# Performance work log

Measured on AMD Instinct MI355X. Metric: run time of the kernel, lower is better.

## Reference

```python
import jax, jax.numpy as jnp
import numpy as np

B, T, C, H = 4, 2048, 1024, 16
HD = C // H

def setup_inputs() -> dict:
    key = jax.random.key(0)
    ks = jax.random.split(key, 9)
    s = 1.0 / np.sqrt(C)
    return {
        'x':  jax.random.normal(ks[0], (B, T, C), jnp.float32),
        'Wq': jax.random.normal(ks[1], (C, C), jnp.float32) * s,
        'bq': jnp.zeros((C,), jnp.float32),
        'Wk': jax.random.normal(ks[2], (C, C), jnp.float32) * s,
        'bk': jnp.zeros((C,), jnp.float32),
        'Wv': jax.random.normal(ks[3], (C, C), jnp.float32) * s,
        'bv': jnp.zeros((C,), jnp.float32),
        'Wo': jax.random.normal(ks[4], (C, C), jnp.float32) * s,
        'bo': jnp.zeros((C,), jnp.float32),
    }

def reference(x, Wq, bq, Wk, bk, Wv, bv, Wo, bo):
    Bx, Tx, Cx = x.shape
    # projections (torch Linear: x @ W.T + b); split heads -> (B,H,T,HD)
    def heads(y):
        return y.reshape(Bx, Tx, H, HD).transpose(0, 2, 1, 3)
    q = heads(x @ Wq.T + bq)
    k = heads(x @ Wk.T + bk)
    v = heads(x @ Wv.T + bv)
    # NOTE: original scales by 1/sqrt(embedding_dim), not head_dim
    scale = 1.0 / jnp.sqrt(jnp.asarray(Cx, x.dtype))
    att = jnp.einsum('bhqd,bhkd->bhqk', q, k) * scale
    mask = jnp.tril(jnp.ones((Tx, Tx), dtype=bool))
    att = jnp.where(mask, att, jnp.asarray(-jnp.inf, att.dtype))
    att = jax.nn.softmax(att, axis=-1)
    y = jnp.einsum('bhqk,bhkd->bhqd', att, v)
    y = y.transpose(0, 2, 1, 3).reshape(Bx, Tx, Cx)
    return y @ Wo.T + bo
```

## Files before the change

### kernel.cpp

```cpp
#include <hip/hip_runtime.h>
#include <hip/hip_bf16.h>
#include <stdint.h>

#define NB 4
#define NT 2048
#define NC 1024
#define NH 16
#define NHD 64
#define NM (NB*NT)

typedef __attribute__((ext_vector_type(8))) __bf16 bf16x8;
typedef __attribute__((ext_vector_type(4))) float floatx4;
typedef __attribute__((ext_vector_type(8))) unsigned short ushortx8;

#define AS1(p) ((const __attribute__((address_space(1))) void*)(p))
#define AS3(p) ((__attribute__((address_space(3))) void*)(p))

__device__ __forceinline__ unsigned short f2bf(float f) {
    union { float f; unsigned int u; } v; v.f = f;
    unsigned int u = v.u;
    return (unsigned short)((u + 0x7FFFu + ((u >> 16) & 1u)) >> 16);
}


__global__ void cast_x_tiled(const float* __restrict__ in,
                             unsigned short* __restrict__ out, int ntiles) {
    const int wid  = (blockIdx.x * blockDim.x + threadIdx.x) >> 6;
    const int lane = threadIdx.x & 63;
    if (wid >= ntiles) return;
    const int R = wid >> 5, C = wid & 31;
    const float* src = in + ((size_t)(R*16 + (lane >> 2)))*1024 + C*32 + (lane & 3)*8;
    const floatx4 v0 = *(const floatx4*)src;
    const floatx4 v1 = *(const floatx4*)(src + 4);
    ushortx8 o;
    o[0] = f2bf(v0[0]); o[1] = f2bf(v0[1]); o[2] = f2bf(v0[2]); o[3] = f2bf(v0[3]);
    o[4] = f2bf(v1[0]); o[5] = f2bf(v1[1]); o[6] = f2bf(v1[2]); o[7] = f2bf(v1[3]);
    *(ushortx8*)&out[(size_t)wid*512 + (((lane & 3)*16 + (lane >> 2)))*8] = o;
}

__global__ void cast4_tiled(const float* __restrict__ w0, const float* __restrict__ w1,
                            const float* __restrict__ w2, const float* __restrict__ w3,
                            unsigned short* __restrict__ o0, unsigned short* __restrict__ o1,
                            unsigned short* __restrict__ o2, unsigned short* __restrict__ o3,
                            int ntiles) {
    const int wid  = (blockIdx.x * blockDim.x + threadIdx.x) >> 6;
    const int lane = threadIdx.x & 63;
    if (wid >= ntiles) return;
    const float* in; unsigned short* out;
    switch (blockIdx.y) {
        case 0: in = w0; out = o0; break;
        case 1: in = w1; out = o1; break;
        case 2: in = w2; out = o2; break;
        default: in = w3; out = o3; break;
    }
    const int R = wid >> 5, C = wid & 31;
    const float* src = in + ((size_t)(R*16 + (lane >> 2)))*1024 + C*32 + (lane & 3)*8;
    const floatx4 v0 = *(const floatx4*)src;
    const floatx4 v1 = *(const floatx4*)(src + 4);
    ushortx8 o;
    o[0] = f2bf(v0[0]); o[1] = f2bf(v0[1]); o[2] = f2bf(v0[2]); o[3] = f2bf(v0[3]);
    o[4] = f2bf(v1[0]); o[5] = f2bf(v1[1]); o[6] = f2bf(v1[2]); o[7] = f2bf(v1[3]);
    *(ushortx8*)&out[(size_t)wid*512 + (((lane & 3)*16 + (lane >> 2)))*8] = o;
}

#define TM 128
#define TN 128
#define BK 32

__device__ __forceinline__ void gemm_core(
    const unsigned short* __restrict__ A,
    const unsigned short* __restrict__ W,
    const float* __restrict__ bias,
    void* __restrict__ Out,
    unsigned short* As, unsigned short* Bs,
    int m_base, int n_base, int N_out, int K, int mode, float oscale)
{
    const int tid  = threadIdx.x;
    const int lane = tid & 63;
    const int wv   = tid >> 6;
    const int quad = lane >> 4;
    const int l16  = lane & 15;
    const int wm = (wv >> 1) * 64;
    const int wn = (wv & 1) * 64;

    floatx4 acc[4][4];
    #pragma unroll
    for (int i = 0; i < 4; ++i)
        #pragma unroll
        for (int j = 0; j < 4; ++j)
            acc[i][j] = (floatx4){0.f, 0.f, 0.f, 0.f};

    const int kTiles = K / BK;
    const int kct = K >> 5;

    const unsigned short* At = A + ((size_t)((m_base >> 4) + wv*2) * kct) * 512 + (size_t)lane*8;
    const unsigned short* Wt = W + ((size_t)((n_base >> 4) + wv*2) * kct) * 512 + (size_t)lane*8;
    const size_t rstride = (size_t)kct * 512;

    for (int kt = 0; kt < kTiles; ++kt) {
        __syncthreads();
        #pragma unroll
        for (int i = 0; i < 2; ++i) {
            __builtin_amdgcn_global_load_lds(
                AS1(At + (size_t)kt*512 + i*rstride),
                AS3(&As[(wv*2 + i)*512]), 16, 0, 0);
            __builtin_amdgcn_global_load_lds(
                AS1(Wt + (size_t)kt*512 + i*rstride),
                AS3(&Bs[(wv*2 + i)*512]), 16, 0, 0);
        }
        __syncthreads();

        bf16x8 af[4], bfr[4];
        #pragma unroll
        for (int mi = 0; mi < 4; ++mi)
            af[mi] = *(const bf16x8*)&As[((wv >> 1)*4 + mi)*512 + lane*8];
        #pragma unroll
        for (int ni = 0; ni < 4; ++ni)
            bfr[ni] = *(const bf16x8*)&Bs[((wv & 1)*4 + ni)*512 + lane*8];

        #pragma unroll
        for (int mi = 0; mi < 4; ++mi)
            #pragma unroll
            for (int ni = 0; ni < 4; ++ni)
                acc[mi][ni] = __builtin_amdgcn_mfma_f32_16x16x32_bf16(
                    af[mi], bfr[ni], acc[mi][ni], 0, 0, 0);
    }

    #pragma unroll
    for (int mi = 0; mi < 4; ++mi) {
        #pragma unroll
        for (int ni = 0; ni < 4; ++ni) {
            const int col = n_base + wn + ni*16 + l16;
            const float bv = bias[col & 1023];
            #pragma unroll
            for (int r = 0; r < 4; ++r) {
                const int row = m_base + wm + mi*16 + quad*4 + r;
                const float v = (acc[mi][ni][r] + bv) * oscale;
                if (mode == 0) {
                    ((float*)Out)[(size_t)row * N_out + col] = v;
                } else if (mode == 1) {
                    const int bb = row >> 11, t = row & (NT - 1);
                    const int h  = (col >> 6) & (NH - 1), d = col & 63;
                    const int bh = bb * NH + h;
                    const size_t idx =
                        ((size_t)((bh*128 + (t >> 4))*2 + (d >> 5)))*512
                        + (size_t)((((d >> 3) & 3)*16 + (t & 15))*8 + (d & 7));
                    ((unsigned short*)Out)[idx] = f2bf(v);
                } else {
                    const int bb = row >> 11, t = row & (NT - 1);
                    const int h  = (col >> 6) & (NH - 1), hd = col & 63;
                    const int bh = bb * NH + h;
                    const size_t idx =
                        ((size_t)((bh*64 + (t >> 5))*4 + (hd >> 4)))*512
                        + (size_t)((((t >> 3) & 3)*16 + (hd & 15))*8 + (t & 7));
                    ((unsigned short*)Out)[idx] = f2bf(v);
                }
            }
        }
    }
}

#define QSCALE (0.03125f * 1.44269504088896340736f)

__global__ __launch_bounds__(256) void gemm_qkv(
    const unsigned short* __restrict__ A,
    const unsigned short* __restrict__ Wq, const unsigned short* __restrict__ Wk,
    const unsigned short* __restrict__ Wv,
    const float* __restrict__ bq, const float* __restrict__ bk,
    const float* __restrict__ bv,
    unsigned short* __restrict__ Qo, unsigned short* __restrict__ Ko,
    unsigned short* __restrict__ Vo)
{
    __shared__ __align__(16) unsigned short As[TM*BK];
    __shared__ __align__(16) unsigned short Bs[TN*BK];
    const int wi = blockIdx.y >> 3;
    const int n_base = (blockIdx.y & 7) * TN;
    const unsigned short* W; const float* bias; void* Out; int mode; float osc;
    if (wi == 0)      { W = Wq; bias = bq; Out = Qo; mode = 1; osc = QSCALE; }
    else if (wi == 1) { W = Wk; bias = bk; Out = Ko; mode = 1; osc = 1.0f; }
    else              { W = Wv; bias = bv; Out = Vo; mode = 2; osc = 1.0f; }
    gemm_core(A, W, bias, Out, As, Bs, blockIdx.x * TM, n_base, NC, NC, mode, osc);
}

__global__ __launch_bounds__(256) void gemm_out(
    const unsigned short* __restrict__ A,
    const unsigned short* __restrict__ W,
    const float* __restrict__ bias,
    float* __restrict__ Out)
{
    __shared__ __align__(16) unsigned short As[TM*BK];
    __shared__ __align__(16) unsigned short Bs[TN*BK];
    gemm_core(A, W, bias, Out, As, Bs, blockIdx.x * TM, blockIdx.y * TN,
              NC, NC, 0, 1.0f);
}

#define LDPP 68

__device__ __forceinline__ void attn_q32(
    const unsigned short* __restrict__ Qf,
    const unsigned short* __restrict__ Kf,
    const unsigned short* __restrict__ Vf,
    unsigned short* __restrict__ Y,
    unsigned short* Pw, int bh, int st, int lane)
{
    const int quad = lane >> 4, l16 = lane & 15;
    const int q0 = st * 32;
    const int b = bh >> 4, h = bh & (NH - 1);

    const size_t qbase = ((size_t)(bh*128 + st*2))*1024 + (size_t)lane*8;
    const bf16x8 qa0 = *(const bf16x8*)&Qf[qbase];
    const bf16x8 qa1 = *(const bf16x8*)&Qf[qbase + 512];
    const bf16x8 qb0 = *(const bf16x8*)&Qf[qbase + 1024];
    const bf16x8 qb1 = *(const bf16x8*)&Qf[qbase + 1536];

    const unsigned short* kp = Kf + (size_t)bh*131072 + (size_t)lane*8;
    const unsigned short* vp = Vf + (size_t)bh*131072 + (size_t)lane*8;

    floatx4 oa[4], ob[4];
    #pragma unroll
    for (int nt = 0; nt < 4; ++nt) {
        oa[nt] = (floatx4){0.f,0.f,0.f,0.f};
        ob[nt] = (floatx4){0.f,0.f,0.f,0.f};
    }
    float la[4] = {0.f,0.f,0.f,0.f}, lb[4] = {0.f,0.f,0.f,0.f};

    const int Ffull = q0 >> 6;

    for (int f = 0; f < Ffull; ++f) {
        const int j0 = f * 64;
        bf16x8 kf[4][2], vf[4][2];
        {
            const unsigned short* kt = kp + (size_t)(j0 >> 4) * 1024;
            #pragma unroll
            for (int ct = 0; ct < 4; ++ct) {
                kf[ct][0] = *(const bf16x8*)&kt[ct*1024];
                kf[ct][1] = *(const bf16x8*)&kt[ct*1024 + 512];
            }
            const unsigned short* vt = vp + (size_t)(j0 >> 5) * 2048;
            #pragma unroll
            for (int nt = 0; nt < 4; ++nt) {
                vf[nt][0] = *(const bf16x8*)&vt[nt*512];
                vf[nt][1] = *(const bf16x8*)&vt[2048 + nt*512];
            }
        }
        {
            floatx4 s[4];
            #pragma unroll
            for (int ct = 0; ct < 4; ++ct) {
                s[ct] = (floatx4){0.f,0.f,0.f,0.f};
                s[ct] = __builtin_amdgcn_mfma_f32_16x16x32_bf16(qa0, kf[ct][0], s[ct], 0,0,0);
                s[ct] = __builtin_amdgcn_mfma_f32_16x16x32_bf16(qa1, kf[ct][1], s[ct], 0,0,0);
            }
            #pragma unroll
            for (int ct = 0; ct < 4; ++ct)
                #pragma unroll
                for (int r = 0; r < 4; ++r) {
                    const float p = __builtin_amdgcn_exp2f(s[ct][r]);
                    la[r] += p;
                    Pw[(quad*4 + r) * LDPP + ct*16 + l16] = f2bf(p);
                }
            const bf16x8 pf0 = *(const bf16x8*)&Pw[l16 * LDPP + quad*8];
            const bf16x8 pf1 = *(const bf16x8*)&Pw[l16 * LDPP + 32 + quad*8];
            #pragma unroll
            for (int nt = 0; nt < 4; ++nt) {
                oa[nt] = __builtin_amdgcn_mfma_f32_16x16x32_bf16(pf0, vf[nt][0], oa[nt], 0,0,0);
                oa[nt] = __builtin_amdgcn_mfma_f32_16x16x32_bf16(pf1, vf[nt][1], oa[nt], 0,0,0);
            }
        }
        {
            floatx4 s[4];
            #pragma unroll
            for (int ct = 0; ct < 4; ++ct) {
                s[ct] = (floatx4){0.f,0.f,0.f,0.f};
                s[ct] = __builtin_amdgcn_mfma_f32_16x16x32_bf16(qb0, kf[ct][0], s[ct], 0,0,0);
                s[ct] = __builtin_amdgcn_mfma_f32_16x16x32_bf16(qb1, kf[ct][1], s[ct], 0,0,0);
            }
            #pragma unroll
            for (int ct = 0; ct < 4; ++ct)
                #pragma unroll
                for (int r = 0; r < 4; ++r) {
                    const float p = __builtin_amdgcn_exp2f(s[ct][r]);
                    lb[r] += p;
                    Pw[(quad*4 + r) * LDPP + ct*16 + l16] = f2bf(p);
                }
            const bf16x8 pf0 = *(const bf16x8*)&Pw[l16 * LDPP + quad*8];
            const bf16x8 pf1 = *(const bf16x8*)&Pw[l16 * LDPP + 32 + quad*8];
            #pragma unroll
            for (int nt = 0; nt < 4; ++nt) {
                ob[nt] = __builtin_amdgcn_mfma_f32_16x16x32_bf16(pf0, vf[nt][0], ob[nt], 0,0,0);
                ob[nt] = __builtin_amdgcn_mfma_f32_16x16x32_bf16(pf1, vf[nt][1], ob[nt], 0,0,0);
            }
        }
    }

    {
        const int j0 = Ffull * 64;
        bf16x8 kf[4][2], vf[4][2];
        {
            const unsigned short* kt = kp + (size_t)(j0 >> 4) * 1024;
            #pragma unroll
            for (int ct = 0; ct < 4; ++ct) {
                kf[ct][0] = *(const bf16x8*)&kt[ct*1024];
                kf[ct][1] = *(const bf16x8*)&kt[ct*1024 + 512];
            }
            const unsigned short* vt = vp + (size_t)(j0 >> 5) * 2048;
            #pragma unroll
            for (int nt = 0; nt < 4; ++nt) {
                vf[nt][0] = *(const bf16x8*)&vt[nt*512];
                vf[nt][1] = *(const bf16x8*)&vt[2048 + nt*512];
            }
        }
        #pragma unroll
        for (int sub = 0; sub < 2; ++sub) {
            const int row_base = q0 + sub*16;
            const bf16x8 qx0 = sub ? qb0 : qa0;
            const bf16x8 qx1 = sub ? qb1 : qa1;
            float* lx = sub ? lb : la;
            floatx4* ox = sub ? ob : oa;
            floatx4 s[4];
            #pragma unroll
            for (int ct = 0; ct < 4; ++ct) {
                s[ct] = (floatx4){0.f,0.f,0.f,0.f};
                s[ct] = __builtin_amdgcn_mfma_f32_16x16x32_bf16(qx0, kf[ct][0], s[ct], 0,0,0);
                s[ct] = __builtin_amdgcn_mfma_f32_16x16x32_bf16(qx1, kf[ct][1], s[ct], 0,0,0);
            }
            #pragma unroll
            for (int ct = 0; ct < 4; ++ct) {
                const int jlo = j0 + ct*16;
                if (jlo >= row_base + 16) {
                    #pragma unroll
                    for (int r = 0; r < 4; ++r)
                        Pw[(quad*4 + r) * LDPP + ct*16 + l16] = 0;
                } else if (jlo + 15 <= row_base) {
                    #pragma unroll
                    for (int r = 0; r < 4; ++r) {
                        const float p = __builtin_amdgcn_exp2f(s[ct][r]);
                        lx[r] += p;
                        Pw[(quad*4 + r) * LDPP + ct*16 + l16] = f2bf(p);
                    }
                } else {
                    #pragma unroll
                    for (int r = 0; r < 4; ++r) {
                        const int j   = jlo + l16;
                        const int row = row_base + quad*4 + r;
                        const float p = (j <= row) ? __builtin_amdgcn_exp2f(s[ct][r]) : 0.f;
                        lx[r] += p;
                        Pw[(quad*4 + r) * LDPP + ct*16 + l16] = f2bf(p);
                    }
                }
            }
            const bf16x8 pf0 = *(const bf16x8*)&Pw[l16 * LDPP + quad*8];
            const bf16x8 pf1 = *(const bf16x8*)&Pw[l16 * LDPP + 32 + quad*8];
            #pragma unroll
            for (int nt = 0; nt < 4; ++nt) {
                ox[nt] = __builtin_amdgcn_mfma_f32_16x16x32_bf16(pf0, vf[nt][0], ox[nt], 0,0,0);
                ox[nt] = __builtin_amdgcn_mfma_f32_16x16x32_bf16(pf1, vf[nt][1], ox[nt], 0,0,0);
            }
        }
    }

    #pragma unroll
    for (int r = 0; r < 4; ++r) {
        float x = la[r];
        x += __shfl_xor(x, 1, 16); x += __shfl_xor(x, 2, 16);
        x += __shfl_xor(x, 4, 16); x += __shfl_xor(x, 8, 16);
        la[r] = 1.0f / x;
        float y = lb[r];
        y += __shfl_xor(y, 1, 16); y += __shfl_xor(y, 2, 16);
        y += __shfl_xor(y, 4, 16); y += __shfl_xor(y, 8, 16);
        lb[r] = 1.0f / y;
    }
    const size_t Rbase = (size_t)((b*NT + q0) >> 4);
    #pragma unroll
    for (int nt = 0; nt < 4; ++nt) {
        const size_t tbase = (Rbase*32 + h*2 + (nt >> 1))*512
                           + (size_t)(((nt & 1)*2 + (l16 >> 3))*128 + (l16 & 7));
        #pragma unroll
        for (int r = 0; r < 4; ++r) {
            const size_t off = tbase + (quad*4 + r)*8;
            Y[off]         = f2bf(oa[nt][r] * la[r]);
            Y[off + 16384] = f2bf(ob[nt][r] * lb[r]);
        }
    }
}

__global__ __launch_bounds__(256) void flash_attn(
    const unsigned short* __restrict__ Qf,
    const unsigned short* __restrict__ Kf,
    const unsigned short* __restrict__ Vf,
    unsigned short* __restrict__ Y)
{
    __shared__ __align__(16) unsigned short Pl[4][16 * LDPP];
    const int tid  = threadIdx.x;
    const int wave = tid >> 6;
    const int lane = tid & 63;
    const int bh = blockIdx.y;
    const int w = blockIdx.x * 4 + wave;
    unsigned short* Pw = &Pl[wave][0];
    attn_q32(Qf, Kf, Vf, Y, Pw, bh, w, lane);
    attn_q32(Qf, Kf, Vf, Y, Pw, bh, 63 - w, lane);
}

extern "C" void kernel_launch(void* const* d_in, const int* in_sizes, int n_in,
                              void* d_out, int out_size, void* d_ws, size_t ws_size,
                              hipStream_t stream) {
    const float* x  = (const float*)d_in[0];
    const float* Wq = (const float*)d_in[1];
    const float* bq = (const float*)d_in[2];
    const float* Wk = (const float*)d_in[3];
    const float* bk = (const float*)d_in[4];
    const float* Wv = (const float*)d_in[5];
    const float* bv = (const float*)d_in[6];
    const float* Wo = (const float*)d_in[7];
    const float* bo = (const float*)d_in[8];

    char* ws = (char*)d_ws;
    size_t off = 0;
    auto alloc = [&](size_t bytes) -> void* {
        void* p = ws + off;
        off += (bytes + 255) & ~(size_t)255;
        return p;
    };
    unsigned short* xb  = (unsigned short*)alloc((size_t)NM * NC * 2);
    unsigned short* Wqb = (unsigned short*)alloc((size_t)NC * NC * 2);
    unsigned short* Wkb = (unsigned short*)alloc((size_t)NC * NC * 2);
    unsigned short* Wvb = (unsigned short*)alloc((size_t)NC * NC * 2);
    unsigned short* Wob = (unsigned short*)alloc((size_t)NC * NC * 2);
    unsigned short* Qb  = (unsigned short*)alloc((size_t)NM * NC * 2);
    unsigned short* Kb  = (unsigned short*)alloc((size_t)NM * NC * 2);
    unsigned short* Vtb = (unsigned short*)alloc((size_t)NM * NC * 2);
    unsigned short* Yb  = (unsigned short*)alloc((size_t)NM * NC * 2);

    const int ntx = NM * NC / 512;
    const int ntw = NC * NC / 512;
    cast_x_tiled<<<(ntx*64 + 255)/256, 256, 0, stream>>>(x, xb, ntx);
    cast4_tiled<<<dim3((ntw*64 + 255)/256, 4), 256, 0, stream>>>(
        Wq, Wk, Wv, Wo, Wqb, Wkb, Wvb, Wob, ntw);

    gemm_qkv<<<dim3(NM / TM, 24), 256, 0, stream>>>(
        xb, Wqb, Wkb, Wvb, bq, bk, bv, Qb, Kb, Vtb);

    flash_attn<<<dim3(8, NB*NH), 256, 0, stream>>>(Qb, Kb, Vtb, Yb);

    gemm_out<<<dim3(NM / TM, NC / TN), 256, 0, stream>>>(Yb, Wob, bo, (float*)d_out);
}
```

Measured before the change: 254.7 us.

## Keep attention probabilities in registers via transposed MFMA, dropping LDS round-trip

Swaps the MFMA operand order so S^T = K·Q^T comes out with the key dimension already in the register layout needed for the P·V product. The exp2 probabilities are packed to bf16 in registers with a byte-permute and fed straight into the PV MFMA, which removes the per-tile LDS write, LDS read and shared buffer. The V tile layout written by the QKV GEMM is permuted to match. The row-sum reduction and output stores are reworked to use vectorized 4-element writes. The diagonal tile is folded into the main loop. This relies on the new V layout and register layout being exactly consistent.

```diff
diff --git a/kernel.cpp b/kernel.cpp
--- a/kernel.cpp
+++ b/kernel.cpp
@@ -20,6 +20,10 @@
     union { float f; unsigned int u; } v; v.f = f;
     unsigned int u = v.u;
     return (unsigned short)((u + 0x7FFFu + ((u >> 16) & 1u)) >> 16);
+}
+__device__ __forceinline__ unsigned int pk2(float lo, float hi) {
+    union { float f; unsigned int u; } a, b; a.f = hi; b.f = lo;
+    return __builtin_amdgcn_perm(a.u, b.u, 0x07060302u);
 }
 
 
@@ -150,9 +154,12 @@
                     const int bb = row >> 11, t = row & (NT - 1);
                     const int h  = (col >> 6) & (NH - 1), hd = col & 63;
                     const int bh = bb * NH + h;
+                    const int tk = t & 31;
+                    const int qv = (tk >> 2) & 3;
+                    const int jv = (tk & 3) + ((tk >> 4) << 2);
                     const size_t idx =
                         ((size_t)((bh*64 + (t >> 5))*4 + (hd >> 4)))*512
-                        + (size_t)((((t >> 3) & 3)*16 + (hd & 15))*8 + (t & 7));
+                        + (size_t)((qv*16 + (hd & 15))*8 + jv);
                     ((unsigned short*)Out)[idx] = f2bf(v);
                 }
             }
@@ -194,14 +201,12 @@
               NC, NC, 0, 1.0f);
 }
 
-#define LDPP 68
-
 __device__ __forceinline__ void attn_q32(
     const unsigned short* __restrict__ Qf,
     const unsigned short* __restrict__ Kf,
     const unsigned short* __restrict__ Vf,
     unsigned short* __restrict__ Y,
-    unsigned short* Pw, int bh, int st, int lane)
+    int bh, int st, int lane)
 {
     const int quad = lane >> 4, l16 = lane & 15;
     const int q0 = st * 32;
@@ -222,12 +227,14 @@
         oa[nt] = (floatx4){0.f,0.f,0.f,0.f};
         ob[nt] = (floatx4){0.f,0.f,0.f,0.f};
     }
-    float la[4] = {0.f,0.f,0.f,0.f}, lb[4] = {0.f,0.f,0.f,0.f};
+    float la = 0.f, lb = 0.f;
 
     const int Ffull = q0 >> 6;
-
-    for (int f = 0; f < Ffull; ++f) {
+    const int ntile = Ffull + 1;
+
+    for (int f = 0; f < ntile; ++f) {
         const int j0 = f * 64;
+        const bool diag = (f == Ffull);
         bf16x8 kf[4][2], vf[4][2];
         {
             const unsigned short* kt = kp + (size_t)(j0 >> 4) * 1024;
@@ -243,144 +250,73 @@
                 vf[nt][1] = *(const bf16x8*)&vt[2048 + nt*512];
             }
         }
-        {
+        #pragma unroll
+        for (int sub = 0; sub < 2; ++sub) {
+            const bf16x8 qx0 = sub ? qb0 : qa0;
+            const bf16x8 qx1 = sub ? qb1 : qa1;
+            floatx4* ox = sub ? ob : oa;
+
             floatx4 s[4];
             #pragma unroll
             for (int ct = 0; ct < 4; ++ct) {
                 s[ct] = (floatx4){0.f,0.f,0.f,0.f};
-                s[ct] = __builtin_amdgcn_mfma_f32_16x16x32_bf16(qa0, kf[ct][0], s[ct], 0,0,0);
-                s[ct] = __builtin_amdgcn_mfma_f32_16x16x32_bf16(qa1, kf[ct][1], s[ct], 0,0,0);
-            }
-            #pragma unroll
-            for (int ct = 0; ct < 4; ++ct)
+                s[ct] = __builtin_amdgcn_mfma_f32_16x16x32_bf16(kf[ct][0], qx0, s[ct], 0,0,0);
+                s[ct] = __builtin_amdgcn_mfma_f32_16x16x32_bf16(kf[ct][1], qx1, s[ct], 0,0,0);
+            }
+            float p[4][4];
+            float lsum = 0.f;
+            if (!diag) {
                 #pragma unroll
-                for (int r = 0; r < 4; ++r) {
-                    const float p = __builtin_amdgcn_exp2f(s[ct][r]);
-                    la[r] += p;
-                    Pw[(quad*4 + r) * LDPP + ct*16 + l16] = f2bf(p);
-                }
-            const bf16x8 pf0 = *(const bf16x8*)&Pw[l16 * LDPP + quad*8];
-            const bf16x8 pf1 = *(const bf16x8*)&Pw[l16 * LDPP + 32 + quad*8];
-            #pragma unroll
-            for (int nt = 0; nt < 4; ++nt) {
-                oa[nt] = __builtin_amdgcn_mfma_f32_16x16x32_bf16(pf0, vf[nt][0], oa[nt], 0,0,0);
-                oa[nt] = __builtin_amdgcn_mfma_f32_16x16x32_bf16(pf1, vf[nt][1], oa[nt], 0,0,0);
-            }
-        }
-        {
-            floatx4 s[4];
-            #pragma unroll
-            for (int ct = 0; ct < 4; ++ct) {
-                s[ct] = (floatx4){0.f,0.f,0.f,0.f};
-                s[ct] = __builtin_amdgcn_mfma_f32_16x16x32_bf16(qb0, kf[ct][0], s[ct], 0,0,0);
-                s[ct] = __builtin_amdgcn_mfma_f32_16x16x32_bf16(qb1, kf[ct][1], s[ct], 0,0,0);
-            }
-            #pragma unroll
-            for (int ct = 0; ct < 4; ++ct)
-                #pragma unroll
-                for (int r = 0; r < 4; ++r) {
-                    const float p = __builtin_amdgcn_exp2f(s[ct][r]);
-                    lb[r] += p;
-                    Pw[(quad*4 + r) * LDPP + ct*16 + l16] = f2bf(p);
-                }
-            const bf16x8 pf0 = *(const bf16x8*)&Pw[l16 * LDPP + quad*8];
-            const bf16x8 pf1 = *(const bf16x8*)&Pw[l16 * LDPP + 32 + quad*8];
-            #pragma unroll
-            for (int nt = 0; nt < 4; ++nt) {
-                ob[nt] = __builtin_amdgcn_mfma_f32_16x16x32_bf16(pf0, vf[nt][0], ob[nt], 0,0,0);
-                ob[nt] = __builtin_amdgcn_mfma_f32_16x16x32_bf16(pf1, vf[nt][1], ob[nt], 0,0,0);
-            }
-        }
-    }
-
-    {
-        const int j0 = Ffull * 64;
-        bf16x8 kf[4][2], vf[4][2];
-        {
-            const unsigned short* kt = kp + (size_t)(j0 >> 4) * 1024;
-            #pragma unroll
-            for (int ct = 0; ct < 4; ++ct) {
-                kf[ct][0] = *(const bf16x8*)&kt[ct*1024];
-                kf[ct][1] = *(const bf16x8*)&kt[ct*1024 + 512];
-            }
-            const unsigned short* vt = vp + (size_t)(j0 >> 5) * 2048;
-            #pragma unroll
-            for (int nt = 0; nt < 4; ++nt) {
-                vf[nt][0] = *(const bf16x8*)&vt[nt*512];
-                vf[nt][1] = *(const bf16x8*)&vt[2048 + nt*512];
-            }
-        }
-        #pragma unroll
-        for (int sub = 0; sub < 2; ++sub) {
-            const int row_base = q0 + sub*16;
-            const bf16x8 qx0 = sub ? qb0 : qa0;
-            const bf16x8 qx1 = sub ? qb1 : qa1;
-            float* lx = sub ? lb : la;
-            floatx4* ox = sub ? ob : oa;
-            floatx4 s[4];
-            #pragma unroll
-            for (int ct = 0; ct < 4; ++ct) {
-                s[ct] = (floatx4){0.f,0.f,0.f,0.f};
-                s[ct] = __builtin_amdgcn_mfma_f32_16x16x32_bf16(qx0, kf[ct][0], s[ct], 0,0,0);
-                s[ct] = __builtin_amdgcn_mfma_f32_16x16x32_bf16(qx1, kf[ct][1], s[ct], 0,0,0);
-            }
-            #pragma unroll
-            for (int ct = 0; ct < 4; ++ct) {
-                const int jlo = j0 + ct*16;
-                if (jlo >= row_base + 16) {
-                    #pragma unroll
-                    for (int r = 0; r < 4; ++r)
-                        Pw[(quad*4 + r) * LDPP + ct*16 + l16] = 0;
-                } else if (jlo + 15 <= row_base) {
+                for (int ct = 0; ct < 4; ++ct)
                     #pragma unroll
                     for (int r = 0; r < 4; ++r) {
-                        const float p = __builtin_amdgcn_exp2f(s[ct][r]);
-                        lx[r] += p;
-                        Pw[(quad*4 + r) * LDPP + ct*16 + l16] = f2bf(p);
+                        p[ct][r] = __builtin_amdgcn_exp2f(s[ct][r]);
+                        lsum += p[ct][r];
                     }
-                } else {
+            } else {
+                const int row = q0 + sub*16 + l16;
+                #pragma unroll
+                for (int ct = 0; ct < 4; ++ct)
                     #pragma unroll
                     for (int r = 0; r < 4; ++r) {
-                        const int j   = jlo + l16;
-                        const int row = row_base + quad*4 + r;
-                        const float p = (j <= row) ? __builtin_amdgcn_exp2f(s[ct][r]) : 0.f;
-                        lx[r] += p;
-                        Pw[(quad*4 + r) * LDPP + ct*16 + l16] = f2bf(p);
+                        const int key = j0 + ct*16 + quad*4 + r;
+                        p[ct][r] = (key <= row) ? __builtin_amdgcn_exp2f(s[ct][r]) : 0.f;
+                        lsum += p[ct][r];
                     }
-                }
-            }
-            const bf16x8 pf0 = *(const bf16x8*)&Pw[l16 * LDPP + quad*8];
-            const bf16x8 pf1 = *(const bf16x8*)&Pw[l16 * LDPP + 32 + quad*8];
+            }
+            if (sub) lb += lsum; else la += lsum;
+
+            union { bf16x8 v; unsigned int u[4]; } pf0, pf1;
+            pf0.u[0] = pk2(p[0][0], p[0][1]); pf0.u[1] = pk2(p[0][2], p[0][3]);
+            pf0.u[2] = pk2(p[1][0], p[1][1]); pf0.u[3] = pk2(p[1][2], p[1][3]);
+            pf1.u[0] = pk2(p[2][0], p[2][1]); pf1.u[1] = pk2(p[2][2], p[2][3]);
+            pf1.u[2] = pk2(p[3][0], p[3][1]); pf1.u[3] = pk2(p[3][2], p[3][3]);
+
             #pragma unroll
             for (int nt = 0; nt < 4; ++nt) {
-                ox[nt] = __builtin_amdgcn_mfma_f32_16x16x32_bf16(pf0, vf[nt][0], ox[nt], 0,0,0);
-                ox[nt] = __builtin_amdgcn_mfma_f32_16x16x32_bf16(pf1, vf[nt][1], ox[nt], 0,0,0);
+                ox[nt] = __builtin_amdgcn_mfma_f32_16x16x32_bf16(vf[nt][0], pf0.v, ox[nt], 0,0,0);
+                ox[nt] = __builtin_amdgcn_mfma_f32_16x16x32_bf16(vf[nt][1], pf1.v, ox[nt], 0,0,0);
             }
         }
     }
 
-    #pragma unroll
-    for (int r = 0; r < 4; ++r) {
-        float x = la[r];
-        x += __shfl_xor(x, 1, 16); x += __shfl_xor(x, 2, 16);
-        x += __shfl_xor(x, 4, 16); x += __shfl_xor(x, 8, 16);
-        la[r] = 1.0f / x;
-        float y = lb[r];
-        y += __shfl_xor(y, 1, 16); y += __shfl_xor(y, 2, 16);
-        y += __shfl_xor(y, 4, 16); y += __shfl_xor(y, 8, 16);
-        lb[r] = 1.0f / y;
-    }
+    la += __shfl_xor(la, 16); la += __shfl_xor(la, 32);
+    lb += __shfl_xor(lb, 16); lb += __shfl_xor(lb, 32);
+    const float ia = 1.0f / la, ib = 1.0f / lb;
+
     const size_t Rbase = (size_t)((b*NT + q0) >> 4);
+    const int cg = (quad >> 1), co = (quad & 1)*4;
     #pragma unroll
     for (int nt = 0; nt < 4; ++nt) {
-        const size_t tbase = (Rbase*32 + h*2 + (nt >> 1))*512
-                           + (size_t)(((nt & 1)*2 + (l16 >> 3))*128 + (l16 & 7));
-        #pragma unroll
-        for (int r = 0; r < 4; ++r) {
-            const size_t off = tbase + (quad*4 + r)*8;
-            Y[off]         = f2bf(oa[nt][r] * la[r]);
-            Y[off + 16384] = f2bf(ob[nt][r] * lb[r]);
-        }
+        const size_t base = ((Rbase*32 + h*2 + (nt >> 1))*512)
+                          + (size_t)((((nt & 1)*2 + cg)*16 + l16)*8 + co);
+        ushort4 wa, wb;
+        wa.x = f2bf(oa[nt][0]*ia); wa.y = f2bf(oa[nt][1]*ia);
+        wa.z = f2bf(oa[nt][2]*ia); wa.w = f2bf(oa[nt][3]*ia);
+        wb.x = f2bf(ob[nt][0]*ib); wb.y = f2bf(ob[nt][1]*ib);
+        wb.z = f2bf(ob[nt][2]*ib); wb.w = f2bf(ob[nt][3]*ib);
+        *(ushort4*)&Y[base]         = wa;
+        *(ushort4*)&Y[base + 16384] = wb;
     }
 }
 
@@ -390,15 +326,13 @@
     const unsigned short* __restrict__ Vf,
     unsigned short* __restrict__ Y)
 {
-    __shared__ __align__(16) unsigned short Pl[4][16 * LDPP];
     const int tid  = threadIdx.x;
     const int wave = tid >> 6;
     const int lane = tid & 63;
     const int bh = blockIdx.y;
     const int w = blockIdx.x * 4 + wave;
-    unsigned short* Pw = &Pl[wave][0];
-    attn_q32(Qf, Kf, Vf, Y, Pw, bh, w, lane);
-    attn_q32(Qf, Kf, Vf, Y, Pw, bh, 63 - w, lane);
+    attn_q32(Qf, Kf, Vf, Y, bh, w, lane);
+    attn_q32(Qf, Kf, Vf, Y, bh, 63 - w, lane);
 }
 
 extern "C" void kernel_launch(void* const* d_in, const int* in_sizes, int n_in,
```

After: 242.4 us. 1.05x faster.
